# Performance work log

Measured on AMD Instinct MI355X. Metric: run time of the kernel, lower is better.

The kernel has to match this reference:

```python
import jax, jax.numpy as jnp
import numpy as np

E = 512
H = 8
HD = E // H
EPS = 1e-5


def setup_inputs() -> dict:
    key = jax.random.key(0)
    ks = jax.random.split(key, 12)
    S, B = 2048, 4
    bound_in = float(np.sqrt(6.0 / (3 * E + E)))  # xavier_uniform for in_proj
    inp = {
        "x": jax.random.normal(ks[0], (S, B, E), dtype=jnp.float32),
        "in_proj_weight": jax.random.uniform(ks[1], (3 * E, E), minval=-bound_in, maxval=bound_in, dtype=jnp.float32),
        "in_proj_bias": jnp.zeros((3 * E,), jnp.float32),
        "out_proj_weight": jax.random.normal(ks[2], (E, E), dtype=jnp.float32) * 0.02,
        "out_proj_bias": jnp.zeros((E,), jnp.float32),
        "ln1_gamma": jnp.ones((E,), jnp.float32),
        "ln1_beta": jnp.zeros((E,), jnp.float32),
        "fc1_weight": jax.random.normal(ks[3], (4 * E, E), dtype=jnp.float32) * 0.02,
        "fc1_bias": jnp.zeros((4 * E,), jnp.float32),
        "fc2_weight": jax.random.normal(ks[4], (E, 4 * E), dtype=jnp.float32) * 0.02,
        "fc2_bias": jnp.zeros((E,), jnp.float32),
        "ln2_gamma": jnp.ones((E,), jnp.float32),
        "ln2_beta": jnp.zeros((E,), jnp.float32),
    }
    return inp


def _layer_norm(x, gamma, beta):
    mu = jnp.mean(x, axis=-1, keepdims=True)
    var = jnp.mean(jnp.square(x - mu), axis=-1, keepdims=True)
    return (x - mu) * jax.lax.rsqrt(var + EPS) * gamma + beta


def _encoder_layer(x, in_w, in_b, out_w, out_b, g1, b1, fc1_w, fc1_b, fc2_w, fc2_b, g2, b2):
    S, B, _ = x.shape
    # --- self attention (hand-rolled, full S x S scores as in original) ---
    qkv = x @ in_w.T + in_b                      # [S, B, 3E]
    q, k, v = jnp.split(qkv, 3, axis=-1)         # each [S, B, E]
    # [S, B, E] -> [B*H, S, HD]
    def to_heads(t):
        return t.reshape(S, B * H, HD).transpose(1, 0, 2)
    q, k, v = to_heads(q), to_heads(k), to_heads(v)
    scores = jnp.einsum('bsd,btd->bst', q, k) / jnp.sqrt(jnp.float32(HD))  # [B*H, S, S]
    attn_w = jax.nn.softmax(scores, axis=-1)
    attn = jnp.einsum('bst,btd->bsd', attn_w, v)  # [B*H, S, HD]
    attn = attn.transpose(1, 0, 2).reshape(S, B, E)
    attn = attn @ out_w.T + out_b
    # --- residual + LN ---
    x = _layer_norm(x + attn, g1, b1)
    # --- FFN ---
    h = jax.nn.relu(x @ fc1_w.T + fc1_b)
    h = h @ fc2_w.T + fc2_b
    return _layer_norm(x + h, g2, b2)


def reference(x, in_proj_weight, in_proj_bias, out_proj_weight, out_proj_bias,
              ln1_gamma, ln1_beta, fc1_weight, fc1_bias, fc2_weight, fc2_bias,
              ln2_gamma, ln2_beta):
    return _encoder_layer(x, in_proj_weight, in_proj_bias, out_proj_weight, out_proj_bias,
                          ln1_gamma, ln1_beta, fc1_weight, fc1_bias, fc2_weight, fc2_bias,
                          ln2_gamma, ln2_beta)
```

## Files before the change

### kernel.cpp

```cpp
#include <hip/hip_runtime.h>

typedef _Float16 half8 __attribute__((ext_vector_type(8)));
typedef _Float16 half4 __attribute__((ext_vector_type(4)));
typedef float f32x4 __attribute__((ext_vector_type(4)));

static __device__ __forceinline__ f32x4 mfma16(half8 a, half8 b, f32x4 c) {
    return __builtin_amdgcn_mfma_f32_16x16x32_f16(a, b, c, 0, 0, 0);
}

static __device__ __forceinline__ void gload16(const void* g, const void* l) {
    __builtin_amdgcn_global_load_lds(
        (const __attribute__((address_space(1))) unsigned int*)(unsigned long long)g,
        (__attribute__((address_space(3))) unsigned int*)(unsigned int)(unsigned long long)l,
        16, 0, 0);
}

__global__ void __launch_bounds__(256) f32_to_f16(const float* __restrict__ in,
                                                  _Float16* __restrict__ out, int n) {
    long i = ((long)blockIdx.x * 256 + threadIdx.x) * 8;
    if (i >= n) return;
    f32x4 v0 = *(const f32x4*)(in + i);
    f32x4 v1 = *(const f32x4*)(in + i + 4);
    half8 h;
#pragma unroll
    for (int j = 0; j < 4; j++) { h[j] = (_Float16)v0[j]; h[4 + j] = (_Float16)v1[j]; }
    *(half8*)(out + i) = h;
}

template <int MODE, int NI>
__global__ void __launch_bounds__(256) gemm_bt(const _Float16* __restrict__ A,
                                               const _Float16* __restrict__ Bw,
                                               const float* __restrict__ bias,
                                               const float* __restrict__ resid,
                                               void* __restrict__ Cout,
                                               int M, int N, int K) {
    constexpr int BN = 32 * NI;
    __shared__ __align__(16) _Float16 As[2][128 * 32];
    __shared__ __align__(16) _Float16 Bs[2][BN * 32];
    const int tid = threadIdx.x;
    const int lane = tid & 63;
    const int w = tid >> 6;
    const int g = lane >> 4, l15 = lane & 15;
    const int wm = w >> 1, wn = w & 1;
    const long rowblk = (long)blockIdx.y * 128;
    const long colblk = (long)blockIdx.x * BN;

    const int lrow = lane >> 2;
    const int lcol = (lane & 3) * 8;

    f32x4 zero = {0.f, 0.f, 0.f, 0.f};
    f32x4 acc[4][NI];
#pragma unroll
    for (int i = 0; i < 4; i++)
#pragma unroll
        for (int j = 0; j < NI; j++) acc[i][j] = zero;

    auto stage = [&](int k0, int buf) {
        gload16(A + (rowblk + w * 32 + lrow) * (long)K + k0 + lcol, As[buf] + w * 1024);
        gload16(A + (rowblk + w * 32 + 16 + lrow) * (long)K + k0 + lcol, As[buf] + w * 1024 + 512);
#pragma unroll
        for (int c = 0; c < NI / 2; c++)
            gload16(Bw + (colblk + w * (8 * NI) + c * 16 + lrow) * (long)K + k0 + lcol,
                    Bs[buf] + w * (8 * NI) * 32 + c * 512);
    };

    stage(0, 0);
    __syncthreads();
    int buf = 0;
    for (int k0 = 0; k0 < K; k0 += 32) {
        if (k0 + 32 < K) stage(k0 + 32, buf ^ 1);
        half8 af[4], bf[NI];
#pragma unroll
        for (int mi = 0; mi < 4; mi++)
            af[mi] = *(const half8*)(As[buf] + (wm * 64 + mi * 16 + l15) * 32 + g * 8);
#pragma unroll
        for (int ni = 0; ni < NI; ni++)
            bf[ni] = *(const half8*)(Bs[buf] + (wn * (16 * NI) + ni * 16 + l15) * 32 + g * 8);
#pragma unroll
        for (int mi = 0; mi < 4; mi++)
#pragma unroll
            for (int ni = 0; ni < NI; ni++)
                acc[mi][ni] = mfma16(af[mi], bf[ni], acc[mi][ni]);
        __syncthreads();
        buf ^= 1;
    }

    const long crow0 = rowblk + wm * 64 + g * 4;
    const long ccol0 = colblk + wn * (16 * NI) + l15;
#pragma unroll
    for (int mi = 0; mi < 4; mi++) {
#pragma unroll
        for (int ni = 0; ni < NI; ni++) {
            const long cc = ccol0 + ni * 16;
            const float bv = bias[cc];
#pragma unroll
            for (int r = 0; r < 4; r++) {
                const long rr = crow0 + mi * 16 + r;
                float v = acc[mi][ni][r] + bv;
                if (MODE == 1) v = fmaxf(v, 0.f);
                if (MODE == 2) {
                    ((float*)Cout)[rr * N + cc] = v + resid[rr * N + cc];
                } else if (MODE == 3) {
                    const long sel = cc >> 9;
                    const int hh = (int)(cc >> 6) & 7;
                    const int dd = (int)cc & 63;
                    const int ss = (int)(rr >> 2), bb = (int)rr & 3;
                    if (sel == 0) v *= 0.18033688f;
                    ((_Float16*)Cout)[sel * (32L * 2048 * 64) +
                                      ((long)(bb * 8 + hh) * 2048 + ss) * 64 + dd] = (_Float16)v;
                } else {
                    ((_Float16*)Cout)[rr * N + cc] = (_Float16)v;
                }
            }
        }
    }
    (void)M;
}

__global__ void __launch_bounds__(256) transpose_v(const _Float16* __restrict__ Vh,
                                                   _Float16* __restrict__ Vt) {
    __shared__ _Float16 T[64][72];
    const int tid = threadIdx.x;
    const int bh = blockIdx.y;
    const int t0 = blockIdx.x * 64;
    const _Float16* src = Vh + ((long)bh * 2048 + t0) * 64;
    const int row = tid >> 2, col = (tid & 3) * 16;
    *(half8*)&T[row][col] = *(const half8*)(src + row * 64 + col);
    *(half8*)&T[row][col + 8] = *(const half8*)(src + row * 64 + col + 8);
    __syncthreads();
    const int d = tid >> 2, tc = (tid & 3) * 16;
    half8 a, b;
#pragma unroll
    for (int j = 0; j < 8; j++) { a[j] = T[tc + j][d]; b[j] = T[tc + 8 + j][d]; }
    _Float16* dst = Vt + ((long)bh * 64 + d) * 2048 + t0 + tc;
    *(half8*)dst = a;
    *(half8*)(dst + 8) = b;
}

__global__ void __launch_bounds__(256) attn_fwd(const _Float16* __restrict__ Qh,
                                                const _Float16* __restrict__ Kh,
                                                const _Float16* __restrict__ Vt,
                                                _Float16* __restrict__ out) {
    __shared__ __align__(16) _Float16 Klds[2][64 * 64];
    __shared__ __align__(16) _Float16 Vlds[2][64 * 64];
    __shared__ __align__(16) _Float16 Plds[4][16 * 64];
    const int tid = threadIdx.x;
    const int lane = tid & 63;
    const int w = tid >> 6;
    const int g = lane >> 4, l15 = lane & 15;
    const int bh = blockIdx.y;
    const int b = bh >> 3, h = bh & 7;
    const int s0 = blockIdx.x * 64 + w * 16;
    const _Float16* Qb = Qh + (long)bh * 2048 * 64;
    const _Float16* Kb = Kh + (long)bh * 2048 * 64;
    const _Float16* Vb = Vt + (long)bh * 64 * 2048;

    const int srow = lane >> 3;
    const int scolb = (lane & 7) * 16;

    half8 qb[2];
#pragma unroll
    for (int ks = 0; ks < 2; ks++)
        qb[ks] = *(const half8*)(Qb + (s0 + l15) * 64 + ks * 32 + g * 8);

    f32x4 zero = {0.f, 0.f, 0.f, 0.f};
    f32x4 ot[4];
#pragma unroll
    for (int di = 0; di < 4; di++) ot[di] = zero;
    float lsum = 0.f;

    auto stage = [&](int t0, int buf) {
#pragma unroll
        for (int j = 0; j < 2; j++) {
            const int row = w * 16 + j * 8 + srow;
            const int src = scolb ^ ((row & 7) << 4);
            gload16(Kb + (long)(t0 + row) * 64 + (src >> 1),
                    Klds[buf] + (w * 16 + j * 8) * 64);
            gload16(Vb + (long)row * 2048 + t0 + (src >> 1),
                    Vlds[buf] + (w * 16 + j * 8) * 64);
        }
    };

    stage(0, 0);
    __syncthreads();
    int buf = 0;

    for (int t0 = 0; t0 < 2048; t0 += 64) {
        if (t0 + 64 < 2048) stage(t0 + 64, buf ^ 1);

        __builtin_amdgcn_s_setprio(1);
        f32x4 st[4];
#pragma unroll
        for (int ni = 0; ni < 4; ni++) {
            st[ni] = zero;
#pragma unroll
            for (int ks = 0; ks < 2; ks++) {
                const int t = ni * 16 + l15;
                const int cb = (ks * 64 + g * 16) ^ ((t & 7) << 4);
                half8 ka = *(const half8*)((const char*)Klds[buf] + t * 128 + cb);
                st[ni] = mfma16(ka, qb[ks], st[ni]);
            }
        }
        __builtin_amdgcn_s_setprio(0);

        char* const pw = (char*)Plds[w] + l15 * 128;
#pragma unroll
        for (int ni = 0; ni < 4; ni++) {
            half4 pv4;
#pragma unroll
            for (int r = 0; r < 4; r++) {
                const float pe = __builtin_exp2f(st[ni][r]);
                lsum += pe;
                pv4[r] = (_Float16)pe;
            }
            *(half4*)(pw + ((ni * 32 + g * 8) ^ ((l15 & 7) << 4))) = pv4;
        }

        half8 pa[2];
#pragma unroll
        for (int ks = 0; ks < 2; ks++)
            pa[ks] = *(const half8*)(pw + ((ks * 64 + g * 16) ^ ((l15 & 7) << 4)));
        __builtin_amdgcn_s_setprio(1);
#pragma unroll
        for (int di = 0; di < 4; di++)
#pragma unroll
            for (int ks = 0; ks < 2; ks++) {
                const int d = di * 16 + l15;
                const int cb = (ks * 64 + g * 16) ^ ((d & 7) << 4);
                half8 vb = *(const half8*)((const char*)Vlds[buf] + d * 128 + cb);
                ot[di] = mfma16(vb, pa[ks], ot[di]);
            }
        __builtin_amdgcn_s_setprio(0);

        __syncthreads();
        buf ^= 1;
    }

    lsum += __shfl_xor(lsum, 16);
    lsum += __shfl_xor(lsum, 32);
    const float inv = 1.f / lsum;
    const long q = s0 + l15;
#pragma unroll
    for (int di = 0; di < 4; di++) {
        half4 hv;
#pragma unroll
        for (int r = 0; r < 4; r++) hv[r] = (_Float16)(ot[di][r] * inv);
        *(half4*)(out + (q * 4 + b) * 512 + h * 64 + di * 16 + g * 4) = hv;
    }
}

__global__ void __launch_bounds__(256) ln_rows(const float* __restrict__ in,
                                               const float* __restrict__ gamma,
                                               const float* __restrict__ beta,
                                               float* __restrict__ outf,
                                               _Float16* __restrict__ outh) {
    const int tid = threadIdx.x, lane = tid & 63, w = tid >> 6;
    const long row = (long)blockIdx.x * 4 + w;
    const float* p = in + row * 512 + lane * 8;
    f32x4 v0 = *(const f32x4*)p;
    f32x4 v1 = *(const f32x4*)(p + 4);
    float s = v0[0] + v0[1] + v0[2] + v0[3] + v1[0] + v1[1] + v1[2] + v1[3];
    float q = v0[0] * v0[0] + v0[1] * v0[1] + v0[2] * v0[2] + v0[3] * v0[3] +
              v1[0] * v1[0] + v1[1] * v1[1] + v1[2] * v1[2] + v1[3] * v1[3];
#pragma unroll
    for (int off = 1; off < 64; off <<= 1) {
        s += __shfl_xor(s, off);
        q += __shfl_xor(q, off);
    }
    const float mu = s * (1.0f / 512.0f);
    const float var = q * (1.0f / 512.0f) - mu * mu;
    const float rstd = rsqrtf(var + 1e-5f);
    const float* gp = gamma + lane * 8;
    const float* bp = beta + lane * 8;
    f32x4 g0 = *(const f32x4*)gp, g1 = *(const f32x4*)(gp + 4);
    f32x4 b0 = *(const f32x4*)bp, b1 = *(const f32x4*)(bp + 4);
    f32x4 o0, o1;
#pragma unroll
    for (int j = 0; j < 4; j++) {
        o0[j] = (v0[j] - mu) * rstd * g0[j] + b0[j];
        o1[j] = (v1[j] - mu) * rstd * g1[j] + b1[j];
    }
    float* op = outf + row * 512 + lane * 8;
    *(f32x4*)op = o0;
    *(f32x4*)(op + 4) = o1;
    if (outh) {
        half8 hh;
#pragma unroll
        for (int j = 0; j < 4; j++) { hh[j] = (_Float16)o0[j]; hh[4 + j] = (_Float16)o1[j]; }
        *(half8*)(outh + row * 512 + lane * 8) = hh;
    }
}

extern "C" void kernel_launch(void* const* d_in, const int* in_sizes, int n_in,
                              void* d_out, int out_size, void* d_ws, size_t ws_size,
                              hipStream_t stream) {
    const float* x    = (const float*)d_in[0];
    const float* inw  = (const float*)d_in[1];
    const float* inb  = (const float*)d_in[2];
    const float* outw = (const float*)d_in[3];
    const float* outb = (const float*)d_in[4];
    const float* g1   = (const float*)d_in[5];
    const float* b1   = (const float*)d_in[6];
    const float* f1w  = (const float*)d_in[7];
    const float* f1b  = (const float*)d_in[8];
    const float* f2w  = (const float*)d_in[9];
    const float* f2b  = (const float*)d_in[10];
    const float* g2   = (const float*)d_in[11];
    const float* b2   = (const float*)d_in[12];

    char* ws = (char*)d_ws;
    const long MB = 1024 * 1024;
    _Float16* X16   = (_Float16*)(ws + 0);
    _Float16* HEADS = (_Float16*)(ws + 8 * MB);
    _Float16* H16   = (_Float16*)(ws + 0);
    _Float16* VT    = (_Float16*)(ws + 32 * MB);
    _Float16* ATT   = (_Float16*)(ws + 40 * MB);
    float*    PRE   = (float*)(ws + 48 * MB);
    float*    YF    = (float*)(ws + 64 * MB);
    _Float16* Y16   = (_Float16*)(ws + 80 * MB);
    _Float16* WIN   = (_Float16*)(ws + 88 * MB);
    _Float16* WOUT  = (_Float16*)(ws + 90 * MB);
    _Float16* WF1   = (_Float16*)(ws + 91 * MB);
    _Float16* WF2   = (_Float16*)(ws + 93 * MB);

    _Float16* Qh = HEADS;
    _Float16* Kh = HEADS + 32L * 2048 * 64;
    _Float16* Vh = HEADS + 2 * 32L * 2048 * 64;

    f32_to_f16<<<2048, 256, 0, stream>>>(x, X16, 8192 * 512);
    f32_to_f16<<<384, 256, 0, stream>>>(inw, WIN, 1536 * 512);
    f32_to_f16<<<128, 256, 0, stream>>>(outw, WOUT, 512 * 512);
    f32_to_f16<<<512, 256, 0, stream>>>(f1w, WF1, 2048 * 512);
    f32_to_f16<<<512, 256, 0, stream>>>(f2w, WF2, 512 * 2048);

    gemm_bt<3, 4><<<dim3(12, 64), 256, 0, stream>>>(X16, WIN, inb, nullptr, HEADS, 8192, 1536, 512);
    transpose_v<<<dim3(32, 32), 256, 0, stream>>>(Vh, VT);
    attn_fwd<<<dim3(32, 32), 256, 0, stream>>>(Qh, Kh, VT, ATT);
    gemm_bt<2, 2><<<dim3(8, 64), 256, 0, stream>>>(ATT, WOUT, outb, x, PRE, 8192, 512, 512);
    ln_rows<<<2048, 256, 0, stream>>>(PRE, g1, b1, YF, Y16);
    gemm_bt<1, 4><<<dim3(16, 64), 256, 0, stream>>>(Y16, WF1, f1b, nullptr, H16, 8192, 2048, 512);
    gemm_bt<2, 2><<<dim3(8, 64), 256, 0, stream>>>(H16, WF2, f2b, YF, PRE, 8192, 512, 2048);
    ln_rows<<<2048, 256, 0, stream>>>(PRE, g2, b2, (float*)d_out, nullptr);
}
```

Baseline: 310.6 us.

## Merge fp16 conversions, relax GEMM waits, vectorize epilogue via swapped MFMA operands

Folds the five fp32-to-fp16 conversion launches into one kernel that picks its source by block index. In the GEMM it swaps the MFMA operands so each lane holds four consecutive output columns, which lets the epilogue use vector bias loads, vector residual loads and vector stores. It also replaces __syncthreads with explicit vmcnt waits plus raw barriers, so the prefetch of the next tile can stay in flight while the current tile is consumed. The hand-written vmcnt counts must match the exact number of issued loads, or the kernel can read stale shared memory.

Result: no change. 305.1 us (-1.8%).

```diff
diff --git a/kernel.cpp b/kernel.cpp
--- a/kernel.cpp
+++ b/kernel.cpp
@@ -15,16 +15,32 @@
         16, 0, 0);
 }
 
-__global__ void __launch_bounds__(256) f32_to_f16(const float* __restrict__ in,
-                                                  _Float16* __restrict__ out, int n) {
-    long i = ((long)blockIdx.x * 256 + threadIdx.x) * 8;
-    if (i >= n) return;
-    f32x4 v0 = *(const f32x4*)(in + i);
-    f32x4 v1 = *(const f32x4*)(in + i + 4);
+__global__ void __launch_bounds__(256) conv_all(const float* __restrict__ x,
+                                                const float* __restrict__ inw,
+                                                const float* __restrict__ outw,
+                                                const float* __restrict__ f1w,
+                                                const float* __restrict__ f2w,
+                                                _Float16* __restrict__ X16,
+                                                _Float16* __restrict__ WIN,
+                                                _Float16* __restrict__ WOUT,
+                                                _Float16* __restrict__ WF1,
+                                                _Float16* __restrict__ WF2) {
+    const int bid = blockIdx.x;
+    const float* src;
+    _Float16* dst;
+    long base;
+    if (bid < 2048)      { src = x;    dst = X16;  base = (long)bid * 2048; }
+    else if (bid < 2432) { src = inw;  dst = WIN;  base = (long)(bid - 2048) * 2048; }
+    else if (bid < 2560) { src = outw; dst = WOUT; base = (long)(bid - 2432) * 2048; }
+    else if (bid < 3072) { src = f1w;  dst = WF1;  base = (long)(bid - 2560) * 2048; }
+    else                 { src = f2w;  dst = WF2;  base = (long)(bid - 3072) * 2048; }
+    const long i = base + threadIdx.x * 8;
+    f32x4 v0 = *(const f32x4*)(src + i);
+    f32x4 v1 = *(const f32x4*)(src + i + 4);
     half8 h;
 #pragma unroll
     for (int j = 0; j < 4; j++) { h[j] = (_Float16)v0[j]; h[4 + j] = (_Float16)v1[j]; }
-    *(half8*)(out + i) = h;
+    *(half8*)(dst + i) = h;
 }
 
 template <int MODE, int NI>
@@ -65,10 +81,16 @@
     };
 
     stage(0, 0);
-    __syncthreads();
     int buf = 0;
     for (int k0 = 0; k0 < K; k0 += 32) {
-        if (k0 + 32 < K) stage(k0 + 32, buf ^ 1);
+        if (k0 + 32 < K) {
+            stage(k0 + 32, buf ^ 1);
+            if constexpr (NI == 4) asm volatile("s_waitcnt vmcnt(4)" ::: "memory");
+            else                   asm volatile("s_waitcnt vmcnt(3)" ::: "memory");
+        } else {
+            asm volatile("s_waitcnt vmcnt(0)" ::: "memory");
+        }
+        __builtin_amdgcn_s_barrier();
         half8 af[4], bf[NI];
 #pragma unroll
         for (int mi = 0; mi < 4; mi++)
@@ -80,37 +102,42 @@
         for (int mi = 0; mi < 4; mi++)
 #pragma unroll
             for (int ni = 0; ni < NI; ni++)
-                acc[mi][ni] = mfma16(af[mi], bf[ni], acc[mi][ni]);
-        __syncthreads();
+                acc[mi][ni] = mfma16(bf[ni], af[mi], acc[mi][ni]);
+        __builtin_amdgcn_s_barrier();
         buf ^= 1;
     }
 
-    const long crow0 = rowblk + wm * 64 + g * 4;
-    const long ccol0 = colblk + wn * (16 * NI) + l15;
 #pragma unroll
     for (int mi = 0; mi < 4; mi++) {
+        const long m = rowblk + wm * 64 + mi * 16 + l15;
 #pragma unroll
         for (int ni = 0; ni < NI; ni++) {
-            const long cc = ccol0 + ni * 16;
-            const float bv = bias[cc];
-#pragma unroll
-            for (int r = 0; r < 4; r++) {
-                const long rr = crow0 + mi * 16 + r;
-                float v = acc[mi][ni][r] + bv;
-                if (MODE == 1) v = fmaxf(v, 0.f);
-                if (MODE == 2) {
-                    ((float*)Cout)[rr * N + cc] = v + resid[rr * N + cc];
-                } else if (MODE == 3) {
-                    const long sel = cc >> 9;
-                    const int hh = (int)(cc >> 6) & 7;
-                    const int dd = (int)cc & 63;
-                    const int ss = (int)(rr >> 2), bb = (int)rr & 3;
-                    if (sel == 0) v *= 0.18033688f;
-                    ((_Float16*)Cout)[sel * (32L * 2048 * 64) +
-                                      ((long)(bb * 8 + hh) * 2048 + ss) * 64 + dd] = (_Float16)v;
-                } else {
-                    ((_Float16*)Cout)[rr * N + cc] = (_Float16)v;
-                }
+            const long n0 = colblk + wn * (16 * NI) + ni * 16 + g * 4;
+            const f32x4 bb = *(const f32x4*)(bias + n0);
+            f32x4 v = acc[mi][ni] + bb;
+            if (MODE == 1) {
+#pragma unroll
+                for (int r = 0; r < 4; r++) v[r] = fmaxf(v[r], 0.f);
+            }
+            if (MODE == 2) {
+                const f32x4 rv = *(const f32x4*)(resid + m * N + n0);
+                *(f32x4*)((float*)Cout + m * N + n0) = v + rv;
+            } else if (MODE == 3) {
+                const long sel = n0 >> 9;
+                const int hh = (int)(n0 >> 6) & 7;
+                const int d0 = (int)n0 & 63;
+                const int ss = (int)(m >> 2), b = (int)m & 3;
+                if (sel == 0) v *= 0.18033688f;
+                half4 hv;
+#pragma unroll
+                for (int r = 0; r < 4; r++) hv[r] = (_Float16)v[r];
+                *(half4*)((_Float16*)Cout + sel * (32L * 2048 * 64) +
+                          ((long)(b * 8 + hh) * 2048 + ss) * 64 + d0) = hv;
+            } else {
+                half4 hv;
+#pragma unroll
+                for (int r = 0; r < 4; r++) hv[r] = (_Float16)v[r];
+                *(half4*)((_Float16*)Cout + m * N + n0) = hv;
             }
         }
     }
@@ -327,11 +354,7 @@
     _Float16* Kh = HEADS + 32L * 2048 * 64;
     _Float16* Vh = HEADS + 2 * 32L * 2048 * 64;
 
-    f32_to_f16<<<2048, 256, 0, stream>>>(x, X16, 8192 * 512);
-    f32_to_f16<<<384, 256, 0, stream>>>(inw, WIN, 1536 * 512);
-    f32_to_f16<<<128, 256, 0, stream>>>(outw, WOUT, 512 * 512);
-    f32_to_f16<<<512, 256, 0, stream>>>(f1w, WF1, 2048 * 512);
-    f32_to_f16<<<512, 256, 0, stream>>>(f2w, WF2, 512 * 2048);
+    conv_all<<<3584, 256, 0, stream>>>(x, inw, outw, f1w, f2w, X16, WIN, WOUT, WF1, WF2);
 
     gemm_bt<3, 4><<<dim3(12, 64), 256, 0, stream>>>(X16, WIN, inb, nullptr, HEADS, 8192, 1536, 512);
     transpose_v<<<dim3(32, 32), 256, 0, stream>>>(Vh, VT);
```
